# Performance work log

Measured on AMD Instinct MI355X. Metric: run time of the kernel, lower is better.

The kernel has to match this reference:

```python
import jax, jax.numpy as jnp
import numpy as np

B, S, D_MODEL, N_HEAD = 8, 512, 1024, 16
HEAD_DIM = D_MODEL // N_HEAD


def _pos_embed(seq_len, dim):
    # RelativeSinusoidalPositionalEmbedding(dim, padding_idx=0, init_size=1200)
    num = 1201  # init_size + 1
    half = dim // 2
    freq = np.exp(np.arange(half, dtype=np.float32) * (-np.log(10000.0) / (half - 1)))
    pos = np.arange(-((num + 1) // 2), num // 2, dtype=np.float32)  # tf.range(-num//2, num//2), python floor div
    emb = pos[:, None] * freq[None, :]
    table = np.concatenate([np.sin(emb), np.cos(emb)], axis=1).astype(np.float32)  # [num, dim]
    table[0] = 0.0  # padding_idx = 0
    origin_shift = num // 2 + 1  # 601
    idx = np.arange(-seq_len, seq_len) + origin_shift
    return jnp.asarray(table[idx])  # [2*seq_len, dim]


def setup_inputs() -> dict:
    key = jax.random.key(0)
    k1, k2, k3, k4 = jax.random.split(key, 4)
    return {
        "x": jax.random.normal(k1, (B, S, D_MODEL), dtype=jnp.float32),
        "mask": jnp.ones((B, S), dtype=jnp.int32),
        "Wqv": jax.random.normal(k2, (D_MODEL, 2 * D_MODEL), dtype=jnp.float32) * 0.02,
        "r_r_bias": jax.random.normal(k3, (N_HEAD, HEAD_DIM), dtype=jnp.float32) * 0.02,
        "r_w_bias": jax.random.normal(k4, (N_HEAD, HEAD_DIM), dtype=jnp.float32) * 0.02,
    }


def _shift(BD):
    # [b, h, s, 2s] -> [b, h, s, s] via pad-reshape trick
    b, h, s, _ = BD.shape
    zp = jnp.zeros((b, h, s, 1), BD.dtype)
    BD = jnp.concatenate([BD, zp], axis=-1).reshape(b, h, 2 * s + 1, s)
    BD = BD[:, :, :-1].reshape(b, h, s, 2 * s)
    return BD[:, :, :, s:]


def reference(x, mask, Wqv, r_r_bias, r_w_bias):
    pos = _pos_embed(S, HEAD_DIM)  # [2S, head_dim], stop-gradient constant
    qv = x @ Wqv  # [B, S, 2*D]
    q, v = jnp.split(qv, 2, axis=-1)

    def heads(t):
        return t.reshape(B, S, N_HEAD, HEAD_DIM).transpose(0, 2, 1, 3)  # bhsd

    q, k, v = heads(q), heads(x), heads(v)
    rw_q = q + r_r_bias[None, :, None, :]
    AC = jnp.einsum('bhqd,bhkd->bhqk', rw_q, k)
    D_ = jnp.einsum('hd,ld->hl', r_w_bias, pos)[None, :, None, :]  # [1, h, 1, 2S]
    B_ = jnp.einsum('bhqd,ld->bhql', q, pos)  # [b, h, S, 2S]
    BD = _shift(B_ + D_)
    attn = AC + BD  # scale=False -> divide by 1
    m = mask.astype(jnp.float32)[:, None, None, :]
    attn = attn * m - (1.0 - m) * 1e8
    attn = jax.nn.softmax(attn, axis=-1)  # dropout is identity at inference
    out = jnp.einsum('bhqk,bhkd->bhqd', attn, v)
    return out.transpose(0, 2, 1, 3).reshape(B, S, D_MODEL)
```

## Files before the change

kernel.cpp:

```cpp
#include <hip/hip_runtime.h>


using h4 = __attribute__((ext_vector_type(4))) _Float16;
using h8 = __attribute__((ext_vector_type(8))) _Float16;
using f32x4 = __attribute__((ext_vector_type(4))) float;

#define MFMA16(a, b, c) __builtin_amdgcn_mfma_f32_16x16x32_f16((a), (b), (c), 0, 0, 0)

#define GLOAD_LDS16(gp, lp)                                                        \
  __builtin_amdgcn_global_load_lds(                                                \
      (const __attribute__((address_space(1))) unsigned int*)(gp),                 \
      (__attribute__((address_space(3))) unsigned int*)(lp), 16, 0, 0)

#define L2E 1.4426950408889634f

__global__ __launch_bounds__(256) void k_prep(const float* __restrict__ x,
                                              const float* __restrict__ Wqv,
                                              _Float16* __restrict__ xh,
                                              _Float16* __restrict__ wT,
                                              _Float16* __restrict__ posP) {
  __shared__ _Float16 t[64][72];
  int bid = blockIdx.x;
  int tid = threadIdx.x;
  if (bid < 2048) {
    size_t idx = (size_t)bid * 256 + tid;
    const float* src = x + idx * 8;
    _Float16 tmp[8];
#pragma unroll
    for (int j = 0; j < 8; ++j) tmp[j] = (_Float16)src[j];
    *(h8*)(xh + idx * 8) = *(const h8*)tmp;
  } else if (bid < 2176) {
    int idx = (bid - 2048) * 256 + tid;
    int tt = idx >> 6, j = idx & 63;
    int jj = j & 31;
    float f = expf((float)jj * (-9.210340371976184f / 31.0f));
    float ang = (float)tt * f;
    posP[idx] = (_Float16)((j < 32) ? sinf(ang) : cosf(ang));
  } else {
    int b2 = bid - 2176;
    int bk = b2 & 15, bn = b2 >> 4;
    int k0 = bk * 64, n0 = bn * 64;
    int r = tid >> 2, c = (tid & 3) * 16;
    const float* src = Wqv + (size_t)(k0 + r) * 2048 + n0 + c;
#pragma unroll
    for (int j = 0; j < 16; ++j) t[r][c + j] = (_Float16)src[j];
    __syncthreads();
    _Float16 tmp[16];
#pragma unroll
    for (int j = 0; j < 16; ++j) tmp[j] = t[c + j][r];
    _Float16* dst = wT + (size_t)(n0 + r) * 1024 + k0 + c;
    *(h8*)dst = *(const h8*)tmp;
    *(h8*)(dst + 8) = *(const h8*)(tmp + 8);
  }
}

__global__ __launch_bounds__(256) void k_gemm(const _Float16* __restrict__ xh,
                                              const _Float16* __restrict__ wT,
                                              const float* __restrict__ rr,
                                              const float* __restrict__ rw,
                                              _Float16* __restrict__ qrr,
                                              _Float16* __restrict__ qrwp,
                                              _Float16* __restrict__ vT) {
  __shared__ _Float16 At[2][128 * 64];
  __shared__ _Float16 Bt[2][128 * 64];

  int bid = blockIdx.x;
  int bm = bid & 31, bn = bid >> 5;
  int tid = threadIdx.x;
  int w = tid >> 6, lane = tid & 63;
  int lr = lane & 15, lg = lane >> 4;

  auto stage = [&](int bufi, int k0) {
#pragma unroll
    for (int it = 0; it < 4; ++it) {
      int a = w * 256 + it * 64 + lane;
      int trow = a >> 3, c8s = (a & 7) ^ (trow & 7);
      GLOAD_LDS16(xh + (size_t)(bm * 128 + trow) * 1024 + k0 + c8s * 8,
                  &At[bufi][a * 8]);
    }
#pragma unroll
    for (int it = 0; it < 4; ++it) {
      int a = w * 256 + it * 64 + lane;
      int trow = a >> 3, c8s = (a & 7) ^ (trow & 7);
      GLOAD_LDS16(wT + (size_t)(bn * 128 + trow) * 1024 + k0 + c8s * 8,
                  &Bt[bufi][a * 8]);
    }
  };

  int wm = w >> 1, wn = w & 1;
  f32x4 acc[4][4] = {};

  stage(0, 0);
  __syncthreads();
  int buf = 0;
  for (int i = 0; i < 16; ++i) {
    if (i < 15) stage(buf ^ 1, (i + 1) * 64);
#pragma unroll
    for (int kk = 0; kk < 2; ++kk) {
      h8 af[4], bf[4];
#pragma unroll
      for (int mi = 0; mi < 4; ++mi) {
        int row = wm * 64 + mi * 16 + lr;
        af[mi] = *(const h8*)(&At[buf][row * 64 + (((kk * 4 + lg) ^ (lr & 7)) * 8)]);
      }
#pragma unroll
      for (int ni = 0; ni < 4; ++ni) {
        int row = wn * 64 + ni * 16 + lr;
        bf[ni] = *(const h8*)(&Bt[buf][row * 64 + (((kk * 4 + lg) ^ (lr & 7)) * 8)]);
      }
#pragma unroll
      for (int mi = 0; mi < 4; ++mi)
#pragma unroll
        for (int ni = 0; ni < 4; ++ni)
          acc[mi][ni] = MFMA16(af[mi], bf[ni], acc[mi][ni]);
    }
    __syncthreads();
    buf ^= 1;
  }

  int hg = bn * 2 + wn;
  int mb = bm * 128 + wm * 64;
  if (hg < 16) {
    int h = hg;
    float rrv[4], rwv[4];
#pragma unroll
    for (int ni = 0; ni < 4; ++ni) {
      rrv[ni] = rr[h * 64 + ni * 16 + lr];
      rwv[ni] = rw[h * 64 + ni * 16 + lr];
    }
    float f0 = expf((float)lr * (-9.210340371976184f / 31.0f));
    float f1 = expf((float)(16 + lr) * (-9.210340371976184f / 31.0f));
#pragma unroll
    for (int mi = 0; mi < 4; ++mi)
#pragma unroll
      for (int r = 0; r < 4; ++r) {
        int m = mb + mi * 16 + lg * 4 + r;
        int b = m >> 9, s = m & 511;
        size_t base = ((size_t)(b * 16 + h) * 512 + s) * 64;
#pragma unroll
        for (int ni = 0; ni < 4; ++ni)
          qrr[base + ni * 16 + lr] = (_Float16)((acc[mi][ni][r] + rrv[ni]) * L2E);
        {
          float qs = acc[mi][0][r] + rwv[0], qc = acc[mi][2][r] + rwv[2];
          float sn, cs;
          __sincosf((float)s * f0, &sn, &cs);
          qrwp[base + lr] = (_Float16)((qs * cs + qc * sn) * L2E);
          qrwp[base + lr + 32] = (_Float16)((qc * cs - qs * sn) * L2E);
        }
        {
          float qs = acc[mi][1][r] + rwv[1], qc = acc[mi][3][r] + rwv[3];
          float sn, cs;
          __sincosf((float)s * f1, &sn, &cs);
          qrwp[base + 16 + lr] = (_Float16)((qs * cs + qc * sn) * L2E);
          qrwp[base + 16 + lr + 32] = (_Float16)((qc * cs - qs * sn) * L2E);
        }
      }
  } else {
    int h = hg - 16;
#pragma unroll
    for (int mi = 0; mi < 4; ++mi) {
      int m = mb + mi * 16 + lg * 4;
      int b = m >> 9, s0 = m & 511;
      size_t vtbase = (size_t)(b * 16 + h) * 64 * 512;
#pragma unroll
      for (int ni = 0; ni < 4; ++ni) {
        int d = ni * 16 + lr;
        _Float16 t4[4];
#pragma unroll
        for (int r = 0; r < 4; ++r) t4[r] = (_Float16)acc[mi][ni][r];
        *(h4*)(vT + vtbase + (size_t)d * 512 + s0) = *(const h4*)t4;
      }
    }
  }
}

__global__ __launch_bounds__(256, 2) void k_attn(const _Float16* __restrict__ xh,
                                                 const _Float16* __restrict__ qrr,
                                                 const _Float16* __restrict__ qrwp,
                                                 const _Float16* __restrict__ vT,
                                                 const _Float16* __restrict__ posPg,
                                                 const int* __restrict__ mask,
                                                 float* __restrict__ out) {
  __shared__ _Float16 Kp[128 * 128];
  __shared__ _Float16 Vt[64 * 128];
  __shared__ _Float16 Pl[4][16 * 136];
  __shared__ float Ma[512];

  int bid = blockIdx.x;
  int qb = bid >> 7, h = bid & 15, b = (bid >> 4) & 7;
  int q0 = qb * 128;
  int tid = threadIdx.x;
  int w = tid >> 6, lane = tid & 63;
  int lr = lane & 15, lg = lane >> 4;

  const size_t bh = (size_t)(b * 16 + h);
  const _Float16* kb = xh + (size_t)b * 512 * 1024 + h * 64;
  const _Float16* vTp = vT + bh * 64 * 512;
  const int* mrow = mask + b * 512;

  auto stage = [&](int t0s) {
#pragma unroll
    for (int it = 0; it < 8; ++it) {
      int a = w * 512 + it * 64 + lane;
      int trow = a >> 4, c16 = a & 15;
      int c16s = c16 ^ (trow & 15);
      const _Float16* g = (c16s < 8)
          ? kb + (size_t)(t0s + trow) * 1024 + c16s * 8
          : posPg + (size_t)(t0s + trow) * 64 + (c16s - 8) * 8;
      GLOAD_LDS16(g, &Kp[(size_t)(w * 512 + it * 64) * 8]);
    }
#pragma unroll
    for (int it = 0; it < 4; ++it) {
      int a = w * 256 + it * 64 + lane;
      int drow = a >> 4, c16 = a & 15;
      int c16s = c16 ^ (drow & 15);
      const _Float16* g = vTp + (size_t)drow * 512 + t0s + c16s * 8;
      GLOAD_LDS16(g, &Vt[(size_t)(w * 256 + it * 64) * 8]);
    }
  };

  Ma[tid] = (1.f - (float)mrow[tid]) * -1.4426950e8f;
  Ma[tid + 256] = (1.f - (float)mrow[tid + 256]) * -1.4426950e8f;

  h8 ar0[2], ar1[2], aw0[2], aw1[2];
#pragma unroll
  for (int rg = 0; rg < 2; ++rg) {
    const _Float16* qrr_p = qrr + (bh * 512 + q0 + 32 * w + 16 * rg + lr) * 64 + lg * 8;
    const _Float16* qrw_p = qrwp + (bh * 512 + q0 + 32 * w + 16 * rg + lr) * 64 + lg * 8;
    ar0[rg] = *(const h8*)(qrr_p);
    ar1[rg] = *(const h8*)(qrr_p + 32);
    aw0[rg] = *(const h8*)(qrw_p);
    aw1[rg] = *(const h8*)(qrw_p + 32);
  }

  float m_run[2] = {-1e30f, -1e30f}, l_run[2] = {0.f, 0.f};
  f32x4 O[2][4];
#pragma unroll
  for (int rg = 0; rg < 2; ++rg)
#pragma unroll
    for (int df = 0; df < 4; ++df) O[rg][df] = (f32x4){0.f, 0.f, 0.f, 0.f};

  _Float16* pw = &Pl[w][0];

  for (int t0 = 0; t0 < 512; t0 += 128) {
    stage(t0);
    __syncthreads();

    float s[2][8][4];
    __builtin_amdgcn_s_setprio(1);
#pragma unroll
    for (int tf = 0; tf < 8; ++tf) {
      int row = tf * 16 + lr;
      const _Float16* bp = &Kp[row * 128];
      h8 b0 = *(const h8*)(bp + ((0 + lg) ^ lr) * 8);
      h8 b1 = *(const h8*)(bp + ((4 + lg) ^ lr) * 8);
      h8 b2 = *(const h8*)(bp + ((8 + lg) ^ lr) * 8);
      h8 b3 = *(const h8*)(bp + ((12 + lg) ^ lr) * 8);
      f32x4 mav = *(const f32x4*)&Ma[t0 + tf * 16 + lg * 4];
#pragma unroll
      for (int rg = 0; rg < 2; ++rg) {
        f32x4 c = {0.f, 0.f, 0.f, 0.f};
        c = MFMA16(b0, ar0[rg], c);
        c = MFMA16(b1, ar1[rg], c);
        c = MFMA16(b2, aw0[rg], c);
        c = MFMA16(b3, aw1[rg], c);
#pragma unroll
        for (int r = 0; r < 4; ++r) s[rg][tf][r] = c[r] + mav[r];
      }
    }
    __builtin_amdgcn_s_setprio(0);

#pragma unroll
    for (int rg = 0; rg < 2; ++rg) {
      float rm = s[rg][0][0];
#pragma unroll
      for (int tf = 0; tf < 8; ++tf)
#pragma unroll
        for (int r = 0; r < 4; ++r) rm = fmaxf(rm, s[rg][tf][r]);
      rm = fmaxf(rm, __shfl_xor(rm, 16));
      rm = fmaxf(rm, __shfl_xor(rm, 32));

      if (!__all(rm - m_run[rg] <= 8.f)) {
        float mn = fmaxf(m_run[rg], rm);
        float sc = exp2f(m_run[rg] - mn);
        m_run[rg] = mn;
        l_run[rg] *= sc;
        float scq[4];
#pragma unroll
        for (int r = 0; r < 4; ++r) scq[r] = __shfl(sc, lg * 4 + r);
#pragma unroll
        for (int df = 0; df < 4; ++df)
#pragma unroll
          for (int r = 0; r < 4; ++r) O[rg][df][r] *= scq[r];
      }

      float rs = 0.f;
#pragma unroll
      for (int tf = 0; tf < 8; ++tf) {
        _Float16 p4[4];
#pragma unroll
        for (int r = 0; r < 4; ++r) {
          float p = exp2f(s[rg][tf][r] - m_run[rg]);
          p4[r] = (_Float16)p;
          rs += (float)p4[r];
        }
        *(h4*)(pw + lr * 136 + tf * 16 + lg * 4) = *(const h4*)p4;
      }
      rs += __shfl_xor(rs, 16);
      rs += __shfl_xor(rs, 32);
      l_run[rg] += rs;

      h8 pa[4];
#pragma unroll
      for (int ks = 0; ks < 4; ++ks)
        pa[ks] = *(const h8*)(pw + lr * 136 + ks * 32 + lg * 8);
      __builtin_amdgcn_s_setprio(1);
#pragma unroll
      for (int df = 0; df < 4; ++df) {
        int row = df * 16 + lr;
        const _Float16* vbp = &Vt[row * 128];
#pragma unroll
        for (int ks = 0; ks < 4; ++ks) {
          h8 vb = *(const h8*)(vbp + ((ks * 4 + lg) ^ lr) * 8);
          O[rg][df] = MFMA16(pa[ks], vb, O[rg][df]);
        }
      }
      __builtin_amdgcn_s_setprio(0);
    }
    __syncthreads();
  }

#pragma unroll
  for (int rg = 0; rg < 2; ++rg) {
    float lq[4];
#pragma unroll
    for (int r = 0; r < 4; ++r) lq[r] = __shfl(l_run[rg], lg * 4 + r);
#pragma unroll
    for (int df = 0; df < 4; ++df)
#pragma unroll
      for (int r = 0; r < 4; ++r) {
        int ii = 32 * w + 16 * rg + lg * 4 + r;
        out[((size_t)b * 512 + q0 + ii) * 1024 + h * 64 + df * 16 + lr] =
            O[rg][df][r] / lq[r];
      }
  }
}

extern "C" void kernel_launch(void* const* d_in, const int* in_sizes, int n_in,
                              void* d_out, int out_size, void* d_ws, size_t ws_size,
                              hipStream_t stream) {
  const float* x = (const float*)d_in[0];
  const int* mask = (const int*)d_in[1];
  const float* Wqv = (const float*)d_in[2];
  const float* rr = (const float*)d_in[3];
  const float* rw = (const float*)d_in[4];
  float* out = (float*)d_out;
  char* ws = (char*)d_ws;
  const size_t MB = 1024 * 1024;
  _Float16* xh = (_Float16*)(ws);
  _Float16* wT = (_Float16*)(ws + 8 * MB);
  _Float16* posP = (_Float16*)(ws + 12 * MB);
  _Float16* qrr = (_Float16*)(ws + 13 * MB);
  _Float16* qrwp = (_Float16*)(ws + 21 * MB);
  _Float16* vT = (_Float16*)(ws + 29 * MB);

  k_prep<<<2688, 256, 0, stream>>>(x, Wqv, xh, wT, posP);
  k_gemm<<<512, 256, 0, stream>>>(xh, wT, rr, rw, qrr, qrwp, vT);
  k_attn<<<512, 256, 0, stream>>>(xh, qrr, qrwp, vT, posP, mask, out);
}
```

Baseline: 68.32 us.

## Double-buffer K/V tiles in attention with 64-key blocks to overlap loads

The attention kernel now processes keys in 64-wide tiles with two LDS buffers, issuing the async global-to-LDS load for the next tile before computing on the current one. This removes one barrier per iteration and lets memory traffic overlap the MFMA and softmax work. LDS footprint is about the same, but there are twice as many iterations, each with more online-softmax rescale checks and less work per barrier. The V swizzle is changed to an 8-chunk XOR pattern to match the narrower rows.

```diff
diff --git a/kernel.cpp b/kernel.cpp
--- a/kernel.cpp
+++ b/kernel.cpp
@@ -181,9 +181,9 @@
                                                  const _Float16* __restrict__ posPg,
                                                  const int* __restrict__ mask,
                                                  float* __restrict__ out) {
-  __shared__ _Float16 Kp[128 * 128];
-  __shared__ _Float16 Vt[64 * 128];
-  __shared__ _Float16 Pl[4][16 * 136];
+  __shared__ _Float16 Kp[2][64 * 128];
+  __shared__ _Float16 Vt[2][64 * 64];
+  __shared__ _Float16 Pl[4][16 * 72];
   __shared__ float Ma[512];
 
   int bid = blockIdx.x;
@@ -198,24 +198,24 @@
   const _Float16* vTp = vT + bh * 64 * 512;
   const int* mrow = mask + b * 512;
 
-  auto stage = [&](int t0s) {
-#pragma unroll
-    for (int it = 0; it < 8; ++it) {
-      int a = w * 512 + it * 64 + lane;
+  auto stage = [&](int bufi, int t0s) {
+#pragma unroll
+    for (int it = 0; it < 4; ++it) {
+      int a = w * 256 + it * 64 + lane;
       int trow = a >> 4, c16 = a & 15;
       int c16s = c16 ^ (trow & 15);
       const _Float16* g = (c16s < 8)
           ? kb + (size_t)(t0s + trow) * 1024 + c16s * 8
           : posPg + (size_t)(t0s + trow) * 64 + (c16s - 8) * 8;
-      GLOAD_LDS16(g, &Kp[(size_t)(w * 512 + it * 64) * 8]);
-    }
-#pragma unroll
-    for (int it = 0; it < 4; ++it) {
-      int a = w * 256 + it * 64 + lane;
-      int drow = a >> 4, c16 = a & 15;
-      int c16s = c16 ^ (drow & 15);
-      const _Float16* g = vTp + (size_t)drow * 512 + t0s + c16s * 8;
-      GLOAD_LDS16(g, &Vt[(size_t)(w * 256 + it * 64) * 8]);
+      GLOAD_LDS16(g, &Kp[bufi][(w * 256 + it * 64) * 8]);
+    }
+#pragma unroll
+    for (int it = 0; it < 2; ++it) {
+      int a = w * 128 + it * 64 + lane;
+      int drow = a >> 3, c8 = a & 7;
+      int c8s = c8 ^ (drow & 7);
+      GLOAD_LDS16(vTp + (size_t)drow * 512 + t0s + c8s * 8,
+                  &Vt[bufi][(w * 128 + it * 64) * 8]);
     }
   };
 
@@ -242,16 +242,19 @@
 
   _Float16* pw = &Pl[w][0];
 
-  for (int t0 = 0; t0 < 512; t0 += 128) {
-    stage(t0);
-    __syncthreads();
-
-    float s[2][8][4];
+  stage(0, 0);
+  __syncthreads();
+  int buf = 0;
+  for (int i = 0; i < 8; ++i) {
+    int t0 = i * 64;
+    if (i < 7) stage(buf ^ 1, t0 + 64);
+
+    float s[2][4][4];
     __builtin_amdgcn_s_setprio(1);
 #pragma unroll
-    for (int tf = 0; tf < 8; ++tf) {
+    for (int tf = 0; tf < 4; ++tf) {
       int row = tf * 16 + lr;
-      const _Float16* bp = &Kp[row * 128];
+      const _Float16* bp = &Kp[buf][row * 128];
       h8 b0 = *(const h8*)(bp + ((0 + lg) ^ lr) * 8);
       h8 b1 = *(const h8*)(bp + ((4 + lg) ^ lr) * 8);
       h8 b2 = *(const h8*)(bp + ((8 + lg) ^ lr) * 8);
@@ -274,7 +277,7 @@
     for (int rg = 0; rg < 2; ++rg) {
       float rm = s[rg][0][0];
 #pragma unroll
-      for (int tf = 0; tf < 8; ++tf)
+      for (int tf = 0; tf < 4; ++tf)
 #pragma unroll
         for (int r = 0; r < 4; ++r) rm = fmaxf(rm, s[rg][tf][r]);
       rm = fmaxf(rm, __shfl_xor(rm, 16));
@@ -296,7 +299,7 @@
 
       float rs = 0.f;
 #pragma unroll
-      for (int tf = 0; tf < 8; ++tf) {
+      for (int tf = 0; tf < 4; ++tf) {
         _Float16 p4[4];
 #pragma unroll
         for (int r = 0; r < 4; ++r) {
@@ -304,30 +307,28 @@
           p4[r] = (_Float16)p;
           rs += (float)p4[r];
         }
-        *(h4*)(pw + lr * 136 + tf * 16 + lg * 4) = *(const h4*)p4;
+        *(h4*)(pw + lr * 72 + tf * 16 + lg * 4) = *(const h4*)p4;
       }
       rs += __shfl_xor(rs, 16);
       rs += __shfl_xor(rs, 32);
       l_run[rg] += rs;
 
-      h8 pa[4];
-#pragma unroll
-      for (int ks = 0; ks < 4; ++ks)
-        pa[ks] = *(const h8*)(pw + lr * 136 + ks * 32 + lg * 8);
+      h8 pa0 = *(const h8*)(pw + lr * 72 + lg * 8);
+      h8 pa1 = *(const h8*)(pw + lr * 72 + 32 + lg * 8);
       __builtin_amdgcn_s_setprio(1);
 #pragma unroll
       for (int df = 0; df < 4; ++df) {
         int row = df * 16 + lr;
-        const _Float16* vbp = &Vt[row * 128];
-#pragma unroll
-        for (int ks = 0; ks < 4; ++ks) {
-          h8 vb = *(const h8*)(vbp + ((ks * 4 + lg) ^ lr) * 8);
-          O[rg][df] = MFMA16(pa[ks], vb, O[rg][df]);
-        }
+        const _Float16* vbp = &Vt[buf][row * 64];
+        h8 vb0 = *(const h8*)(vbp + ((0 + lg) ^ (lr & 7)) * 8);
+        h8 vb1 = *(const h8*)(vbp + ((4 + lg) ^ (lr & 7)) * 8);
+        O[rg][df] = MFMA16(pa0, vb0, O[rg][df]);
+        O[rg][df] = MFMA16(pa1, vb1, O[rg][df]);
       }
       __builtin_amdgcn_s_setprio(0);
     }
     __syncthreads();
+    buf ^= 1;
   }
 
 #pragma unroll
```

Result: slower. 70.02 us (+2.5%).
